# Optimization experiments

Hardware: AMD Instinct MI355X
Metric: run time of the kernel (lower is better)

Reference implementation:

```python
import jax, jax.numpy as jnp
import numpy as np

N, E = 100000, 1600000
HID, N_CHUNKS, STRU = 128, 8, 4


def setup_inputs() -> dict:
    key = jax.random.key(0)
    ks = jax.random.split(key, 7)
    x = jax.random.normal(ks[0], (N, HID), dtype=jnp.float32)
    e = jax.random.randint(ks[1], (2, E), 0, N, dtype=jnp.int64)
    ratio = jax.random.uniform(ks[2], (), dtype=jnp.float32)
    out_w = N_CHUNKS * STRU
    Wq = jax.random.normal(ks[3], (out_w, HID), dtype=jnp.float32) / np.sqrt(HID)
    bq = jax.random.normal(ks[4], (out_w,), dtype=jnp.float32) * 0.01
    Wv = jax.random.normal(ks[5], (out_w, HID), dtype=jnp.float32) / np.sqrt(HID)
    bv = jax.random.normal(ks[6], (out_w,), dtype=jnp.float32) * 0.01
    return {"x": x, "e": e, "ratio": ratio, "Wq": Wq, "bq": bq, "Wv": Wv, "bv": bv}


def reference(x, e, ratio, Wq, bq, Wv, bv):
    # edge-indexed gather of endpoint features: [E, HID]
    eu = x[e[0]]
    ev = x[e[1]]
    # two linear projections, elementwise multiply: [E, STRU*N_CHUNKS]
    ku = eu @ Wq.T + bq
    kv = ev @ Wv.T + bv
    ks = ku * kv
    # hsplit(STRU) -> STRU contiguous chunks of width N_CHUNKS; sum each chunk
    sums = ks.reshape(E, STRU, N_CHUNKS).sum(axis=-1)  # [E, STRU]
    w = jax.nn.sigmoid(sums) * (1.0 - ratio) * 0.5 + 1.0
    # original returns a list of STRU arrays of shape [E]; stack for a single output
    return jnp.transpose(w)  # [STRU, E]
```

## Files before the change

kernel.cpp:

```cpp
#include <hip/hip_runtime.h>
#include <hip/hip_bf16.h>
#include <cstddef>

constexpr int HID  = 128;
constexpr int OUTW = 32;
constexpr int TOT  = 64;
constexpr int STRU = 4;
constexpr int NCH  = 8;

typedef short  bf16x8 __attribute__((ext_vector_type(8)));
typedef float  f32x4  __attribute__((ext_vector_type(4)));
typedef int    int4v  __attribute__((ext_vector_type(4)));

__device__ __forceinline__ unsigned short f2bf(float f) {
    unsigned u = __builtin_bit_cast(unsigned, f);
    u += 0x7FFFu + ((u >> 16) & 1u);
    return (unsigned short)(u >> 16);
}

__device__ __forceinline__ float dot4(float4 a, float4 b) {
    return a.x * b.x + a.y * b.y + a.z * b.z + a.w * b.w;
}

__global__ __launch_bounds__(256) void prep_bf16(
    const float* __restrict__ Wq, const float* __restrict__ bq,
    const float* __restrict__ Wv, const float* __restrict__ bv,
    unsigned short* __restrict__ Wb, float* __restrict__ bias)
{
    int tid = blockIdx.x * blockDim.x + threadIdx.x;
    if (tid < TOT * HID) {
        int o = tid >> 7, k = tid & 127;
        float w = (o < OUTW) ? Wq[o * HID + k] : Wv[(o - OUTW) * HID + k];
        Wb[tid] = f2bf(w);
    }
    if (tid < TOT) bias[tid] = (tid < OUTW) ? bq[tid] : bv[tid - OUTW];
}

__global__ __launch_bounds__(256) void proj_mfma(
    const float* __restrict__ x,
    const unsigned short* __restrict__ Wb,
    const float* __restrict__ bias,
    unsigned short* __restrict__ P,
    unsigned short* __restrict__ Q,
    int n_nodes)
{
    const int wid  = threadIdx.x >> 6;
    const int lane = threadIdx.x & 63;
    const int lr   = lane & 15;
    const int lg   = lane >> 4;
    const int m0   = blockIdx.x * 64 + wid * 16;

    bf16x8 bfrag[4][4];
#pragma unroll
    for (int t = 0; t < 4; ++t)
#pragma unroll
        for (int kc = 0; kc < 4; ++kc)
            bfrag[t][kc] = *reinterpret_cast<const bf16x8*>(
                Wb + ((size_t)(t * 16 + lr) * HID + kc * 32 + lg * 8));

    f32x4 acc[4];
#pragma unroll
    for (int t = 0; t < 4; ++t) {
        float b = bias[t * 16 + lr];
        acc[t][0] = b; acc[t][1] = b; acc[t][2] = b; acc[t][3] = b;
    }

    const int  arow = m0 + lr;
    const bool aok  = arow < n_nodes;
    const float* ap = x + (size_t)arow * HID;

#pragma unroll
    for (int kc = 0; kc < 4; ++kc) {
        float4 f0 = make_float4(0.f, 0.f, 0.f, 0.f), f1 = f0;
        if (aok) {
            const float4* p = reinterpret_cast<const float4*>(ap + kc * 32 + lg * 8);
            f0 = p[0]; f1 = p[1];
        }
        bf16x8 a;
        a[0] = (short)f2bf(f0.x); a[1] = (short)f2bf(f0.y);
        a[2] = (short)f2bf(f0.z); a[3] = (short)f2bf(f0.w);
        a[4] = (short)f2bf(f1.x); a[5] = (short)f2bf(f1.y);
        a[6] = (short)f2bf(f1.z); a[7] = (short)f2bf(f1.w);
#pragma unroll
        for (int t = 0; t < 4; ++t)
            acc[t] = __builtin_amdgcn_mfma_f32_16x16x32_bf16(a, bfrag[t][kc], acc[t], 0, 0, 0);
    }

    const int mrow = m0 + lg * 4;
#pragma unroll
    for (int j = 0; j < 4; ++j) {
        int node = mrow + j;
        if (node < n_nodes) {
#pragma unroll
            for (int t = 0; t < 4; ++t) {
                unsigned short v = f2bf(acc[t][j]);
                if (t < 2) P[(size_t)node * OUTW + t * 16 + lr] = v;
                else       Q[(size_t)node * OUTW + (t - 2) * 16 + lr] = v;
            }
        }
    }
}

__global__ __launch_bounds__(256) void edge_bf16(
    const int* __restrict__ e,
    const unsigned short* __restrict__ P,
    const unsigned short* __restrict__ Q,
    const float* __restrict__ ratio_p,
    float* __restrict__ out, int E_)
{
    int i = blockIdx.x * blockDim.x + threadIdx.x;
    if (i >= E_) return;

    float scale = (1.0f - ratio_p[0]) * 0.5f;
    int e0 = e[i];
    int e1 = e[E_ + i];

    const int4v* p4 = reinterpret_cast<const int4v*>(P + (size_t)e0 * OUTW);
    const int4v* q4 = reinterpret_cast<const int4v*>(Q + (size_t)e1 * OUTW);

#pragma unroll
    for (int s = 0; s < STRU; ++s) {
        int4v a = p4[s];
        int4v b = q4[s];
        float sum = 0.f;
#pragma unroll
        for (int w = 0; w < 4; ++w) {
            float alo = __builtin_bit_cast(float, (unsigned)(a[w] << 16));
            float ahi = __builtin_bit_cast(float, (unsigned)a[w] & 0xffff0000u);
            float blo = __builtin_bit_cast(float, (unsigned)(b[w] << 16));
            float bhi = __builtin_bit_cast(float, (unsigned)b[w] & 0xffff0000u);
            sum = fmaf(alo, blo, sum);
            sum = fmaf(ahi, bhi, sum);
        }
        float sig = 1.0f / (1.0f + __expf(-sum));
        out[(size_t)s * E_ + i] = sig * scale + 1.0f;
    }
}

__global__ __launch_bounds__(256) void fused_kernel(
    const float* __restrict__ x,
    const int* __restrict__ e,
    const float* __restrict__ ratio_p,
    const float* __restrict__ Wq, const float* __restrict__ bq,
    const float* __restrict__ Wv, const float* __restrict__ bv,
    float* __restrict__ out, int E_)
{
    int i = blockIdx.x * blockDim.x + threadIdx.x;
    if (i >= E_) return;

    float scale = (1.0f - ratio_p[0]) * 0.5f;
    int e0 = e[i];
    int e1 = e[E_ + i];

    const float4* __restrict__ xu  = reinterpret_cast<const float4*>(x + (size_t)e0 * HID);
    const float4* __restrict__ xv_ = reinterpret_cast<const float4*>(x + (size_t)e1 * HID);
    const float4* __restrict__ Wq4 = reinterpret_cast<const float4*>(Wq);
    const float4* __restrict__ Wv4 = reinterpret_cast<const float4*>(Wv);

#pragma unroll 1
    for (int s = 0; s < STRU; ++s) {
        float accP[NCH], accQ[NCH];
#pragma unroll
        for (int c = 0; c < NCH; ++c) { accP[c] = bq[s*NCH+c]; accQ[c] = bv[s*NCH+c]; }
        for (int kc = 0; kc < HID / 4; ++kc) {
            float4 u = xu[kc];
            float4 v = xv_[kc];
#pragma unroll
            for (int c = 0; c < NCH; ++c) {
                int o = s * NCH + c;
                accP[c] += dot4(u, Wq4[o * (HID / 4) + kc]);
                accQ[c] += dot4(v, Wv4[o * (HID / 4) + kc]);
            }
        }
        float sum = 0.0f;
#pragma unroll
        for (int c = 0; c < NCH; ++c) sum += accP[c] * accQ[c];
        float sig = 1.0f / (1.0f + __expf(-sum));
        out[(size_t)s * E_ + i] = sig * scale + 1.0f;
    }
}

extern "C" void kernel_launch(void* const* d_in, const int* in_sizes, int n_in,
                              void* d_out, int out_size, void* d_ws, size_t ws_size,
                              hipStream_t stream)
{
    const float* x     = (const float*)d_in[0];
    const int*   e     = (const int*)  d_in[1];
    const float* ratio = (const float*)d_in[2];
    const float* Wq    = (const float*)d_in[3];
    const float* bq    = (const float*)d_in[4];
    const float* Wv    = (const float*)d_in[5];
    const float* bv    = (const float*)d_in[6];
    float* out = (float*)d_out;

    int N_ = in_sizes[0] / HID;
    int E_ = in_sizes[1] / 2;

    size_t need = (size_t)N_ * OUTW * 2 * sizeof(unsigned short)
                + (size_t)TOT * HID * sizeof(unsigned short)
                + TOT * sizeof(float);
    if (ws_size >= need) {
        unsigned short* P    = (unsigned short*)d_ws;
        unsigned short* Qb   = P + (size_t)N_ * OUTW;
        unsigned short* Wb   = Qb + (size_t)N_ * OUTW;
        float*          bias = (float*)(Wb + (size_t)TOT * HID);

        prep_bf16<<<(TOT * HID + 255) / 256, 256, 0, stream>>>(Wq, bq, Wv, bv, Wb, bias);
        proj_mfma<<<(N_ + 63) / 64, 256, 0, stream>>>(x, Wb, bias, P, Qb, N_);
        edge_bf16<<<(E_ + 255) / 256, 256, 0, stream>>>(e, P, Qb, ratio, out, E_);
    } else {
        fused_kernel<<<(E_ + 255) / 256, 256, 0, stream>>>(x, e, ratio, Wq, bq, Wv, bv, out, E_);
    }
}
```

Measured before the change: 77.84 us.

## Interleave P/Q into one buffer, stage projection stores via LDS, two edges per thread

The separate P and Q bf16 tables become a single interleaved PQ table of 64 values per node, and the projection kernel stages its MFMA outputs in shared memory so it can write them out as coalesced 16-byte vector stores. The edge kernel now handles two edges per thread, using vector loads for the indices and float2 stores for the outputs, and issues all gathers before computing. The goal is fewer scattered 2-byte stores, better memory-level parallelism in the gathers, and less per-edge overhead. The interleaved layout doubles the row stride of each gathered half, so cache-line use per gather may drop, and each thread now holds more registers.

```diff
diff --git a/kernel.cpp b/kernel.cpp
--- a/kernel.cpp
+++ b/kernel.cpp
@@ -11,6 +11,7 @@
 typedef short  bf16x8 __attribute__((ext_vector_type(8)));
 typedef float  f32x4  __attribute__((ext_vector_type(4)));
 typedef int    int4v  __attribute__((ext_vector_type(4)));
+typedef unsigned short u16x8 __attribute__((ext_vector_type(8)));
 
 __device__ __forceinline__ unsigned short f2bf(float f) {
     unsigned u = __builtin_bit_cast(unsigned, f);
@@ -20,6 +21,19 @@
 
 __device__ __forceinline__ float dot4(float4 a, float4 b) {
     return a.x * b.x + a.y * b.y + a.z * b.z + a.w * b.w;
+}
+
+__device__ __forceinline__ float bfdot(int4v a, int4v b, float sum) {
+#pragma unroll
+    for (int w = 0; w < 4; ++w) {
+        float alo = __builtin_bit_cast(float, (unsigned)(a[w] << 16));
+        float ahi = __builtin_bit_cast(float, (unsigned)a[w] & 0xffff0000u);
+        float blo = __builtin_bit_cast(float, (unsigned)(b[w] << 16));
+        float bhi = __builtin_bit_cast(float, (unsigned)b[w] & 0xffff0000u);
+        sum = fmaf(alo, blo, sum);
+        sum = fmaf(ahi, bhi, sum);
+    }
+    return sum;
 }
 
 __global__ __launch_bounds__(256) void prep_bf16(
@@ -40,15 +54,17 @@
     const float* __restrict__ x,
     const unsigned short* __restrict__ Wb,
     const float* __restrict__ bias,
-    unsigned short* __restrict__ P,
-    unsigned short* __restrict__ Q,
+    unsigned short* __restrict__ PQ,
     int n_nodes)
 {
+    __shared__ unsigned short sPQ[64][TOT + 8];
+
     const int wid  = threadIdx.x >> 6;
     const int lane = threadIdx.x & 63;
     const int lr   = lane & 15;
     const int lg   = lane >> 4;
-    const int m0   = blockIdx.x * 64 + wid * 16;
+    const int base = blockIdx.x * 64;
+    const int m0   = base + wid * 16;
 
     bf16x8 bfrag[4][4];
 #pragma unroll
@@ -86,54 +102,73 @@
             acc[t] = __builtin_amdgcn_mfma_f32_16x16x32_bf16(a, bfrag[t][kc], acc[t], 0, 0, 0);
     }
 
-    const int mrow = m0 + lg * 4;
-#pragma unroll
-    for (int j = 0; j < 4; ++j) {
-        int node = mrow + j;
-        if (node < n_nodes) {
-#pragma unroll
-            for (int t = 0; t < 4; ++t) {
-                unsigned short v = f2bf(acc[t][j]);
-                if (t < 2) P[(size_t)node * OUTW + t * 16 + lr] = v;
-                else       Q[(size_t)node * OUTW + (t - 2) * 16 + lr] = v;
-            }
-        }
+    const int lrow = wid * 16 + lg * 4;
+#pragma unroll
+    for (int t = 0; t < 4; ++t)
+#pragma unroll
+        for (int j = 0; j < 4; ++j)
+            sPQ[lrow + j][t * 16 + lr] = f2bf(acc[t][j]);
+    __syncthreads();
+
+    const int row  = threadIdx.x >> 2;
+    const int cseg = (threadIdx.x & 3) * 16;
+    const int node = base + row;
+    if (node < n_nodes) {
+        u16x8 v0 = *reinterpret_cast<const u16x8*>(&sPQ[row][cseg]);
+        u16x8 v1 = *reinterpret_cast<const u16x8*>(&sPQ[row][cseg + 8]);
+        u16x8* dst = reinterpret_cast<u16x8*>(PQ + (size_t)node * TOT + cseg);
+        dst[0] = v0;
+        dst[1] = v1;
     }
 }
 
 __global__ __launch_bounds__(256) void edge_bf16(
     const int* __restrict__ e,
-    const unsigned short* __restrict__ P,
-    const unsigned short* __restrict__ Q,
+    const unsigned short* __restrict__ PQ,
     const float* __restrict__ ratio_p,
     float* __restrict__ out, int E_)
 {
-    int i = blockIdx.x * blockDim.x + threadIdx.x;
+    int i = (blockIdx.x * blockDim.x + threadIdx.x) * 2;
     if (i >= E_) return;
 
     float scale = (1.0f - ratio_p[0]) * 0.5f;
-    int e0 = e[i];
-    int e1 = e[E_ + i];
-
-    const int4v* p4 = reinterpret_cast<const int4v*>(P + (size_t)e0 * OUTW);
-    const int4v* q4 = reinterpret_cast<const int4v*>(Q + (size_t)e1 * OUTW);
-
+    const bool two = (i + 1 < E_);
+
+    int e0a, e0b, e1a, e1b;
+    if (two) {
+        int2 ea = *reinterpret_cast<const int2*>(e + i);
+        int2 eb = *reinterpret_cast<const int2*>(e + E_ + i);
+        e0a = ea.x; e0b = ea.y; e1a = eb.x; e1b = eb.y;
+    } else {
+        e0a = e0b = e[i];
+        e1a = e1b = e[E_ + i];
+    }
+
+    const int4v* pA = reinterpret_cast<const int4v*>(PQ + (size_t)e0a * TOT);
+    const int4v* pB = reinterpret_cast<const int4v*>(PQ + (size_t)e0b * TOT);
+    const int4v* qA = reinterpret_cast<const int4v*>(PQ + (size_t)e1a * TOT + OUTW);
+    const int4v* qB = reinterpret_cast<const int4v*>(PQ + (size_t)e1b * TOT + OUTW);
+
+    int4v a0[STRU], b0[STRU], a1[STRU], b1[STRU];
 #pragma unroll
     for (int s = 0; s < STRU; ++s) {
-        int4v a = p4[s];
-        int4v b = q4[s];
-        float sum = 0.f;
-#pragma unroll
-        for (int w = 0; w < 4; ++w) {
-            float alo = __builtin_bit_cast(float, (unsigned)(a[w] << 16));
-            float ahi = __builtin_bit_cast(float, (unsigned)a[w] & 0xffff0000u);
-            float blo = __builtin_bit_cast(float, (unsigned)(b[w] << 16));
-            float bhi = __builtin_bit_cast(float, (unsigned)b[w] & 0xffff0000u);
-            sum = fmaf(alo, blo, sum);
-            sum = fmaf(ahi, bhi, sum);
+        a0[s] = pA[s];
+        b0[s] = qA[s];
+        a1[s] = pB[s];
+        b1[s] = qB[s];
+    }
+
+#pragma unroll
+    for (int s = 0; s < STRU; ++s) {
+        float s0 = bfdot(a0[s], b0[s], 0.f);
+        float s1 = bfdot(a1[s], b1[s], 0.f);
+        float r0 = 1.0f / (1.0f + __expf(-s0)) * scale + 1.0f;
+        float r1 = 1.0f / (1.0f + __expf(-s1)) * scale + 1.0f;
+        if (two) {
+            *reinterpret_cast<float2*>(out + (size_t)s * E_ + i) = make_float2(r0, r1);
+        } else {
+            out[(size_t)s * E_ + i] = r0;
         }
-        float sig = 1.0f / (1.0f + __expf(-sum));
-        out[(size_t)s * E_ + i] = sig * scale + 1.0f;
     }
 }
 
@@ -196,18 +231,18 @@
     int N_ = in_sizes[0] / HID;
     int E_ = in_sizes[1] / 2;
 
-    size_t need = (size_t)N_ * OUTW * 2 * sizeof(unsigned short)
+    size_t need = (size_t)N_ * TOT * sizeof(unsigned short)
                 + (size_t)TOT * HID * sizeof(unsigned short)
                 + TOT * sizeof(float);
     if (ws_size >= need) {
-        unsigned short* P    = (unsigned short*)d_ws;
-        unsigned short* Qb   = P + (size_t)N_ * OUTW;
-        unsigned short* Wb   = Qb + (size_t)N_ * OUTW;
+        unsigned short* PQ   = (unsigned short*)d_ws;
+        unsigned short* Wb   = PQ + (size_t)N_ * TOT;
         float*          bias = (float*)(Wb + (size_t)TOT * HID);
 
         prep_bf16<<<(TOT * HID + 255) / 256, 256, 0, stream>>>(Wq, bq, Wv, bv, Wb, bias);
-        proj_mfma<<<(N_ + 63) / 64, 256, 0, stream>>>(x, Wb, bias, P, Qb, N_);
-        edge_bf16<<<(E_ + 255) / 256, 256, 0, stream>>>(e, P, Qb, ratio, out, E_);
+        proj_mfma<<<(N_ + 63) / 64, 256, 0, stream>>>(x, Wb, bias, PQ, N_);
+        int nthread = (E_ + 1) / 2;
+        edge_bf16<<<(nthread + 255) / 256, 256, 0, stream>>>(e, PQ, ratio, out, E_);
     } else {
         fused_kernel<<<(E_ + 255) / 256, 256, 0, stream>>>(x, e, ratio, Wq, bq, Wv, bv, out, E_);
     }
```

Result: slower. 87.07 us (+11.9%).

## Stage projection outputs through LDS for vector stores and use nontemporal edge loads

Applied to the files above, without the earlier changes.

The projection kernel now loads all x rows up front with nontemporal loads. It writes the MFMA results into a padded LDS tile and then emits 16-byte coalesced stores of P and Q instead of scattered 2-byte stores. The edge kernel issues all gather loads before computing and uses nontemporal loads for indices and nontemporal stores for outputs, to cut write transactions and keep streamed data out of cache. This adds an LDS buffer and a barrier, and may raise register pressure.

```diff
diff --git a/kernel.cpp b/kernel.cpp
--- a/kernel.cpp
+++ b/kernel.cpp
@@ -11,6 +11,7 @@
 typedef short  bf16x8 __attribute__((ext_vector_type(8)));
 typedef float  f32x4  __attribute__((ext_vector_type(4)));
 typedef int    int4v  __attribute__((ext_vector_type(4)));
+typedef unsigned short u16x8 __attribute__((ext_vector_type(8)));
 
 __device__ __forceinline__ unsigned short f2bf(float f) {
     unsigned u = __builtin_bit_cast(unsigned, f);
@@ -20,6 +21,19 @@
 
 __device__ __forceinline__ float dot4(float4 a, float4 b) {
     return a.x * b.x + a.y * b.y + a.z * b.z + a.w * b.w;
+}
+
+__device__ __forceinline__ float bfdot(int4v a, int4v b, float sum) {
+#pragma unroll
+    for (int w = 0; w < 4; ++w) {
+        float alo = __builtin_bit_cast(float, (unsigned)(a[w] << 16));
+        float ahi = __builtin_bit_cast(float, (unsigned)a[w] & 0xffff0000u);
+        float blo = __builtin_bit_cast(float, (unsigned)(b[w] << 16));
+        float bhi = __builtin_bit_cast(float, (unsigned)b[w] & 0xffff0000u);
+        sum = fmaf(alo, blo, sum);
+        sum = fmaf(ahi, bhi, sum);
+    }
+    return sum;
 }
 
 __global__ __launch_bounds__(256) void prep_bf16(
@@ -44,11 +58,31 @@
     unsigned short* __restrict__ Q,
     int n_nodes)
 {
+    __shared__ unsigned short sPQ[64][TOT + 8];
+
     const int wid  = threadIdx.x >> 6;
     const int lane = threadIdx.x & 63;
     const int lr   = lane & 15;
     const int lg   = lane >> 4;
-    const int m0   = blockIdx.x * 64 + wid * 16;
+    const int base = blockIdx.x * 64;
+    const int m0   = base + wid * 16;
+
+    const int  arow = m0 + lr;
+    const bool aok  = arow < n_nodes;
+    const float* ap = x + (size_t)arow * HID;
+
+    f32x4 xv[8];
+#pragma unroll
+    for (int kc = 0; kc < 4; ++kc) {
+        if (aok) {
+            const f32x4* p = reinterpret_cast<const f32x4*>(ap + kc * 32 + lg * 8);
+            xv[2 * kc + 0] = __builtin_nontemporal_load(p);
+            xv[2 * kc + 1] = __builtin_nontemporal_load(p + 1);
+        } else {
+            xv[2 * kc + 0] = (f32x4)0.f;
+            xv[2 * kc + 1] = (f32x4)0.f;
+        }
+    }
 
     bf16x8 bfrag[4][4];
 #pragma unroll
@@ -65,39 +99,39 @@
         acc[t][0] = b; acc[t][1] = b; acc[t][2] = b; acc[t][3] = b;
     }
 
-    const int  arow = m0 + lr;
-    const bool aok  = arow < n_nodes;
-    const float* ap = x + (size_t)arow * HID;
-
 #pragma unroll
     for (int kc = 0; kc < 4; ++kc) {
-        float4 f0 = make_float4(0.f, 0.f, 0.f, 0.f), f1 = f0;
-        if (aok) {
-            const float4* p = reinterpret_cast<const float4*>(ap + kc * 32 + lg * 8);
-            f0 = p[0]; f1 = p[1];
-        }
+        f32x4 f0 = xv[2 * kc + 0], f1 = xv[2 * kc + 1];
         bf16x8 a;
-        a[0] = (short)f2bf(f0.x); a[1] = (short)f2bf(f0.y);
-        a[2] = (short)f2bf(f0.z); a[3] = (short)f2bf(f0.w);
-        a[4] = (short)f2bf(f1.x); a[5] = (short)f2bf(f1.y);
-        a[6] = (short)f2bf(f1.z); a[7] = (short)f2bf(f1.w);
+        a[0] = (short)f2bf(f0[0]); a[1] = (short)f2bf(f0[1]);
+        a[2] = (short)f2bf(f0[2]); a[3] = (short)f2bf(f0[3]);
+        a[4] = (short)f2bf(f1[0]); a[5] = (short)f2bf(f1[1]);
+        a[6] = (short)f2bf(f1[2]); a[7] = (short)f2bf(f1[3]);
 #pragma unroll
         for (int t = 0; t < 4; ++t)
             acc[t] = __builtin_amdgcn_mfma_f32_16x16x32_bf16(a, bfrag[t][kc], acc[t], 0, 0, 0);
     }
 
-    const int mrow = m0 + lg * 4;
-#pragma unroll
-    for (int j = 0; j < 4; ++j) {
-        int node = mrow + j;
-        if (node < n_nodes) {
-#pragma unroll
-            for (int t = 0; t < 4; ++t) {
-                unsigned short v = f2bf(acc[t][j]);
-                if (t < 2) P[(size_t)node * OUTW + t * 16 + lr] = v;
-                else       Q[(size_t)node * OUTW + (t - 2) * 16 + lr] = v;
-            }
-        }
+    const int lrow = wid * 16 + lg * 4;
+#pragma unroll
+    for (int t = 0; t < 4; ++t)
+#pragma unroll
+        for (int j = 0; j < 4; ++j)
+            sPQ[lrow + j][t * 16 + lr] = f2bf(acc[t][j]);
+    __syncthreads();
+
+    const int row  = threadIdx.x >> 2;
+    const int q    = threadIdx.x & 3;
+    const int node = base + row;
+    if (node < n_nodes) {
+        const int scol = q * 16;
+        u16x8 v0 = *reinterpret_cast<const u16x8*>(&sPQ[row][scol]);
+        u16x8 v1 = *reinterpret_cast<const u16x8*>(&sPQ[row][scol + 8]);
+        unsigned short* dstbase = (q < 2) ? (P + (size_t)node * OUTW + q * 16)
+                                          : (Q + (size_t)node * OUTW + (q - 2) * 16);
+        u16x8* dst = reinterpret_cast<u16x8*>(dstbase);
+        dst[0] = v0;
+        dst[1] = v1;
     }
 }
 
@@ -112,28 +146,22 @@
     if (i >= E_) return;
 
     float scale = (1.0f - ratio_p[0]) * 0.5f;
-    int e0 = e[i];
-    int e1 = e[E_ + i];
+    int e0 = __builtin_nontemporal_load(e + i);
+    int e1 = __builtin_nontemporal_load(e + E_ + i);
 
     const int4v* p4 = reinterpret_cast<const int4v*>(P + (size_t)e0 * OUTW);
     const int4v* q4 = reinterpret_cast<const int4v*>(Q + (size_t)e1 * OUTW);
 
+    int4v a[STRU], b[STRU];
+#pragma unroll
+    for (int s = 0; s < STRU; ++s) { a[s] = p4[s]; b[s] = q4[s]; }
+
 #pragma unroll
     for (int s = 0; s < STRU; ++s) {
-        int4v a = p4[s];
-        int4v b = q4[s];
-        float sum = 0.f;
-#pragma unroll
-        for (int w = 0; w < 4; ++w) {
-            float alo = __builtin_bit_cast(float, (unsigned)(a[w] << 16));
-            float ahi = __builtin_bit_cast(float, (unsigned)a[w] & 0xffff0000u);
-            float blo = __builtin_bit_cast(float, (unsigned)(b[w] << 16));
-            float bhi = __builtin_bit_cast(float, (unsigned)b[w] & 0xffff0000u);
-            sum = fmaf(alo, blo, sum);
-            sum = fmaf(ahi, bhi, sum);
-        }
+        float sum = bfdot(a[s], b[s], 0.f);
         float sig = 1.0f / (1.0f + __expf(-sum));
-        out[(size_t)s * E_ + i] = sig * scale + 1.0f;
+        float r   = sig * scale + 1.0f;
+        __builtin_nontemporal_store(r, out + (size_t)s * E_ + i);
     }
 }
 
```

New measurement: 84.61 us. 1.09x slower.
